# Kernel tuning notes

Hardware: AMD Instinct MI355X
Metric: run time of the kernel (lower is better)

Reference implementation:

```python
import jax, jax.numpy as jnp
import numpy as np


def setup_inputs() -> dict:
    key = jax.random.key(0)
    k_x, k_w = jax.random.split(key)
    S, B, D, H = 2048, 16, 1024, 1024
    X = jax.random.normal(k_x, (S, B, D), dtype=jnp.float32)
    hidden = jnp.zeros((B, H), dtype=jnp.float32)  # initial C_0
    W = jax.random.normal(k_w, (3 * H, D), dtype=jnp.float32) * 0.02
    b = jnp.zeros((3 * H,), dtype=jnp.float32)
    return {"X": X, "hidden": hidden, "W": W, "b": b}


def reference(X, hidden, W, b):
    # QRNNLayer forward, window=1, output_gate=True, zoneout off (eval).
    # Linear projection: [S,B,D] @ [D,3H] -> [S,B,3H]
    Y = jnp.einsum('sbd,hd->sbh', X, W) + b
    Z, F, O = jnp.split(Y, 3, axis=2)
    Z = jnp.tanh(Z)
    F = jax.nn.sigmoid(F)
    O = jax.nn.sigmoid(O)

    # ForgetMult fo-pool: C_t = F_t * Z_t + (1 - F_t) * C_{t-1}
    def step(c, fz):
        f, z = fz
        c = f * z + (1.0 - f) * c
        return c, c

    _, C = jax.lax.scan(step, hidden, (F, Z))  # C: [S,B,H]
    H_out = O * C
    return H_out, C[-1:, :, :]  # (H, last cell state [1,B,H])
```

## Files before the change

kernel.cpp:

```cpp
#include <hip/hip_runtime.h>
#include <hip/hip_bf16.h>
#include <cstdint>
#include <cstddef>

#define S_LEN 2048
#define BATCH 16
#define DIM   1024
#define HID   1024
#define M_TOT (S_LEN * BATCH)
#define N_TOT (3 * HID)
#define K_TOT DIM
#define NCHUNK 32
#define CHLEN (S_LEN / NCHUNK)

#define BM 256
#define BN 256
#define BK 64
#define NT (K_TOT / BK)
#define NITER (NT / 2)
#define GRID_M (M_TOT / BM)
#define GRID_N (N_TOT / BN)
#define NWG (GRID_M * GRID_N)

typedef __bf16 bf16x8 __attribute__((ext_vector_type(8)));
typedef float  f32x4  __attribute__((ext_vector_type(4)));

__device__ __forceinline__ unsigned short f2bf(float f) {
    unsigned int u = __float_as_uint(f);
    u += 0x7FFFu + ((u >> 16) & 1u);
    return (unsigned short)(u >> 16);
}
__device__ __forceinline__ float bf2f(unsigned int s) {
    return __uint_as_float(s << 16);
}
__device__ __forceinline__ float fast_sigmoid(float x) { return 1.0f / (1.0f + __expf(-x)); }
__device__ __forceinline__ float fast_tanh(float x)    { return 2.0f / (1.0f + __expf(-2.0f * x)) - 1.0f; }

__global__ void __launch_bounds__(256) cvt_f32_bf16(const float* __restrict__ in,
                                                    unsigned short* __restrict__ out, int n4) {
    int i = blockIdx.x * blockDim.x + threadIdx.x;
    const int stride = gridDim.x * blockDim.x;
    for (; i < n4; i += stride) {
        const float4 v = reinterpret_cast<const float4*>(in)[i];
        ushort4 o;
        o.x = f2bf(v.x); o.y = f2bf(v.y); o.z = f2bf(v.z); o.w = f2bf(v.w);
        reinterpret_cast<ushort4*>(out)[i] = o;
    }
}

#define GLOAD_LDS16(gp, lp)                                                         \
    __builtin_amdgcn_global_load_lds((__attribute__((address_space(1))) void*)(gp), \
                                     (__attribute__((address_space(3))) void*)(lp), 16, 0, 0)

__global__ void __launch_bounds__(512, 2)
gemm_gates(const unsigned short* __restrict__ Xb,
           const unsigned short* __restrict__ Wb,
           const float* __restrict__ bias,
           unsigned short* __restrict__ gates) {
    __shared__ __align__(16) unsigned short LDSbuf[4 * BM * BK];
#define AS(s) (LDSbuf + (s) * (BM * BK))
#define BS(s) (LDSbuf + 2 * (BM * BK) + (s) * (BN * BK))

    const int tid  = threadIdx.x;
    const int lane = tid & 63;
    const int wid  = tid >> 6;
    const int wm   = wid >> 2;
    const int wn   = wid & 3;
    const int lr   = lane & 15;
    const int lc   = (lane >> 4) & 3;

    const int swz = (blockIdx.x & 7) * (NWG / 8) + (blockIdx.x >> 3);
    const int bn = swz % GRID_N;
    const int bm = swz / GRID_N;

    const int srow  = tid >> 3;
    const int scolE = (((tid & 7) ^ ((tid >> 3) & 7)) << 3);
    const unsigned short* gAs = Xb + (size_t)(bm * BM + srow) * K_TOT + scolE;
    const unsigned short* gBs = Wb + (size_t)(bn * BN + srow) * K_TOT + scolE;

#define STAGE_A(T, q) GLOAD_LDS16(gAs + (size_t)(q) * 64 * K_TOT + (T) * BK, \
                                  AS((T) & 1) + (q) * 4096 + tid * 8)
#define STAGE_B(T, q) GLOAD_LDS16(gBs + (size_t)(q) * 64 * K_TOT + (T) * BK, \
                                  BS((T) & 1) + (q) * 4096 + tid * 8)

#define LDA(dst, s, mf, kw) do { const int _r = wm * 128 + (mf) * 16 + lr;            \
        dst = *reinterpret_cast<const bf16x8*>(                                        \
            AS(s) + _r * 64 + (((((kw) << 2) | lc) ^ (_r & 7)) << 3)); } while (0)
#define LDB(dst, s, nf, kw) do { const int _r = wn * 64 + (nf) * 16 + lr;             \
        dst = *reinterpret_cast<const bf16x8*>(                                        \
            BS(s) + _r * 64 + (((((kw) << 2) | lc) ^ (_r & 7)) << 3)); } while (0)

#define RD_A(s, MH) do { _Pragma("unroll") for (int mi = 0; mi < 4; ++mi) {           \
        LDA(a[mi][0], s, (MH) * 4 + mi, 0); LDA(a[mi][1], s, (MH) * 4 + mi, 1); } } while (0)
#define RD_B(dst, s, NH) do { _Pragma("unroll") for (int ni = 0; ni < 2; ++ni) {      \
        LDB(dst[ni][0], s, (NH) * 2 + ni, 0); LDB(dst[ni][1], s, (NH) * 2 + ni, 1); } } while (0)

#define MM16(A_, B_, M0, N0) do {                                                     \
    _Pragma("unroll") for (int mi = 0; mi < 4; ++mi)                                  \
    _Pragma("unroll") for (int ni = 0; ni < 2; ++ni) {                                \
        acc[(M0) + mi][(N0) + ni] = __builtin_amdgcn_mfma_f32_16x16x32_bf16(          \
            A_[mi][0], B_[ni][0], acc[(M0) + mi][(N0) + ni], 0, 0, 0);                \
        acc[(M0) + mi][(N0) + ni] = __builtin_amdgcn_mfma_f32_16x16x32_bf16(          \
            A_[mi][1], B_[ni][1], acc[(M0) + mi][(N0) + ni], 0, 0, 0);                \
    } } while (0)

#define BAR __builtin_amdgcn_s_barrier()
#define SP1 __builtin_amdgcn_s_setprio(1)
#define SP0 __builtin_amdgcn_s_setprio(0)

    f32x4 acc[8][4];
#pragma unroll
    for (int m = 0; m < 8; ++m)
#pragma unroll
        for (int n = 0; n < 4; ++n) acc[m][n] = {0.0f, 0.0f, 0.0f, 0.0f};

    bf16x8 a[4][2], b[2][2], b2[2][2];

    STAGE_A(0, 0); STAGE_A(0, 1); STAGE_A(0, 2); STAGE_A(0, 3);
    STAGE_B(0, 0); STAGE_B(0, 1); STAGE_B(0, 2); STAGE_B(0, 3);
    STAGE_A(1, 0); STAGE_A(1, 2);
    STAGE_B(1, 0); STAGE_B(1, 1);
    STAGE_A(1, 1); STAGE_A(1, 3);
    asm volatile("s_waitcnt vmcnt(6)" ::: "memory");
    BAR;

#pragma unroll 1
    for (int j = 0; j < NITER; ++j) {
        const int t0 = 2 * j;
        const int t1 = 2 * j + 1;
        const bool st = (j < NITER - 1);
        RD_A(0, 0); RD_B(b, 0, 0);
        STAGE_B(t1, 2); STAGE_B(t1, 3);
        BAR; SP1; MM16(a, b, 0, 0); SP0; BAR;
        RD_B(b2, 0, 1);
        if (st) { STAGE_A(t0 + 2, 0); STAGE_A(t0 + 2, 2); }
        BAR; SP1; MM16(a, b2, 0, 2); SP0; BAR;
        RD_A(0, 1);
        if (st) { STAGE_B(t0 + 2, 0); STAGE_B(t0 + 2, 1); }
        BAR; SP1; MM16(a, b, 4, 0); SP0; BAR;
        if (st) { STAGE_A(t0 + 2, 1); STAGE_A(t0 + 2, 3); }
        BAR; SP1; MM16(a, b2, 4, 2); SP0;
        if (st) asm volatile("s_waitcnt vmcnt(6)" ::: "memory");
        else    asm volatile("s_waitcnt vmcnt(0)" ::: "memory");
        BAR;
        RD_A(1, 0); RD_B(b, 1, 0);
        if (st) { STAGE_B(t0 + 2, 2); STAGE_B(t0 + 2, 3); }
        BAR; SP1; MM16(a, b, 0, 0); SP0; BAR;
        RD_B(b2, 1, 1);
        if (st) { STAGE_A(t1 + 2, 0); STAGE_A(t1 + 2, 2); }
        BAR; SP1; MM16(a, b2, 0, 2); SP0; BAR;
        RD_A(1, 1);
        if (st) { STAGE_B(t1 + 2, 0); STAGE_B(t1 + 2, 1); }
        BAR; SP1; MM16(a, b, 4, 0); SP0; BAR;
        if (st) { STAGE_A(t1 + 2, 1); STAGE_A(t1 + 2, 3); }
        BAR; SP1; MM16(a, b2, 4, 2); SP0;
        if (st) asm volatile("s_waitcnt vmcnt(6)" ::: "memory");
        BAR;
    }
#undef STAGE_A
#undef STAGE_B
#undef LDA
#undef LDB
#undef RD_A
#undef RD_B
#undef MM16
#undef BAR
#undef SP1
#undef SP0

    const int gate_id = bn >> 2;
    {
        const int rl0 = wm * 128 + ((lane >> 4) << 2);
        const int cl0 = wn * 64 + lr;
#pragma unroll
        for (int nf = 0; nf < 4; ++nf) {
            const int col = cl0 + nf * 16;
            const float bb = bias[bn * BN + col];
#pragma unroll
            for (int mf = 0; mf < 8; ++mf) {
#pragma unroll
                for (int r = 0; r < 4; ++r) {
                    const int row = rl0 + mf * 16 + r;
                    const float y = acc[mf][nf][r] + bb;
                    const float g = (gate_id == 0) ? fast_tanh(y) : fast_sigmoid(y);
                    const int phys = (col >> 3) ^ (row & 7);
                    LDSbuf[row * 256 + (phys << 3) + (col & 7)] = f2bf(g);
                }
            }
        }
    }
    __syncthreads();
    {
        const int gr  = lane & 31;
        const int rsub = lane >> 5;
#pragma unroll
        for (int i = 0; i < 16; ++i) {
            const int rl  = wid * 32 + i * 2 + rsub;
            const int phys = gr ^ (rl & 7);
            const bf16x8 v = *reinterpret_cast<const bf16x8*>(&LDSbuf[rl * 256 + (phys << 3)]);
            *reinterpret_cast<bf16x8*>(&gates[(size_t)(bm * BM + rl) * N_TOT + bn * BN + gr * 8]) = v;
        }
    }
#undef AS
#undef BS
}

__global__ void __launch_bounds__(256) scan_phase1(const unsigned short* __restrict__ gates,
                                                   float* __restrict__ Aprod,
                                                   float* __restrict__ Cend) {
    const int t = blockIdx.x * 256 + threadIdx.x;
    const int hp = t & 511;
    const int b  = (t >> 9) & (BATCH - 1);
    const int chunk = t >> 13;
    float c0 = 0.f, c1 = 0.f, a0 = 1.f, a1 = 1.f;
    const int m0 = chunk * (CHLEN * BATCH) + b;
    const unsigned short* gz = gates + (size_t)m0 * N_TOT + hp * 2;
#pragma unroll 4
    for (int i = 0; i < CHLEN; ++i) {
        const unsigned short* p = gz + (size_t)i * BATCH * N_TOT;
        const unsigned int zz = *reinterpret_cast<const unsigned int*>(p);
        const unsigned int ff = *reinterpret_cast<const unsigned int*>(p + HID);
        const float z0 = bf2f(zz & 0xffffu), z1 = bf2f(zz >> 16);
        const float f0 = bf2f(ff & 0xffffu), f1 = bf2f(ff >> 16);
        const float o0 = 1.f - f0, o1 = 1.f - f1;
        c0 = f0 * z0 + o0 * c0;  c1 = f1 * z1 + o1 * c1;
        a0 *= o0;                a1 *= o1;
    }
    const int idx = chunk * (BATCH * HID) + b * HID + hp * 2;
    *reinterpret_cast<float2*>(&Aprod[idx]) = make_float2(a0, a1);
    *reinterpret_cast<float2*>(&Cend[idx])  = make_float2(c0, c1);
}

__global__ void __launch_bounds__(256) scan_combine(const float* __restrict__ Aprod,
                                                    const float* __restrict__ Cend,
                                                    const float* __restrict__ hidden,
                                                    float* __restrict__ Cstart,
                                                    float* __restrict__ c_last) {
    const int t = blockIdx.x * 256 + threadIdx.x;
    float c = hidden[t];
#pragma unroll
    for (int j = 0; j < NCHUNK; ++j) {
        const int idx = j * (BATCH * HID) + t;
        Cstart[idx] = c;
        c = Aprod[idx] * c + Cend[idx];
    }
    c_last[t] = c;
}

__global__ void __launch_bounds__(256) scan_phase3(const unsigned short* __restrict__ gates,
                                                   const float* __restrict__ Cstart,
                                                   float* __restrict__ Hout) {
    const int t = blockIdx.x * 256 + threadIdx.x;
    const int hp = t & 511;
    const int b  = (t >> 9) & (BATCH - 1);
    const int chunk = t >> 13;
    const int idx = chunk * (BATCH * HID) + b * HID + hp * 2;
    float2 cs = *reinterpret_cast<const float2*>(&Cstart[idx]);
    float c0 = cs.x, c1 = cs.y;
    const int m0 = chunk * (CHLEN * BATCH) + b;
    const unsigned short* gz = gates + (size_t)m0 * N_TOT + hp * 2;
#pragma unroll 4
    for (int i = 0; i < CHLEN; ++i) {
        const unsigned short* p = gz + (size_t)i * BATCH * N_TOT;
        const unsigned int zz = *reinterpret_cast<const unsigned int*>(p);
        const unsigned int ff = *reinterpret_cast<const unsigned int*>(p + HID);
        const unsigned int oo = *reinterpret_cast<const unsigned int*>(p + 2 * HID);
        const float z0 = bf2f(zz & 0xffffu), z1 = bf2f(zz >> 16);
        const float f0 = bf2f(ff & 0xffffu), f1 = bf2f(ff >> 16);
        const float g0 = bf2f(oo & 0xffffu), g1 = bf2f(oo >> 16);
        c0 = f0 * z0 + (1.f - f0) * c0;
        c1 = f1 * z1 + (1.f - f1) * c1;
        const int m = m0 + i * BATCH;
        *reinterpret_cast<float2*>(&Hout[(size_t)m * HID + hp * 2]) = make_float2(g0 * c0, g1 * c1);
    }
}

extern "C" void kernel_launch(void* const* d_in, const int* in_sizes, int n_in,
                              void* d_out, int out_size, void* d_ws, size_t ws_size,
                              hipStream_t stream) {
    const float* X      = (const float*)d_in[0];
    const float* hidden = (const float*)d_in[1];
    const float* W      = (const float*)d_in[2];
    const float* bias   = (const float*)d_in[3];
    float* out    = (float*)d_out;
    float* c_last = out + (size_t)M_TOT * HID;

    char* ws = (char*)d_ws;
    unsigned short* Xb    = (unsigned short*)ws;
    unsigned short* Wb    = (unsigned short*)(ws + (size_t)M_TOT * K_TOT * 2);
    unsigned short* gates = Wb + (size_t)N_TOT * K_TOT;
    float* Aprod  = (float*)(gates + (size_t)M_TOT * N_TOT);
    float* Cend   = Aprod + (size_t)NCHUNK * BATCH * HID;
    float* Cstart = Cend  + (size_t)NCHUNK * BATCH * HID;

    cvt_f32_bf16<<<dim3(2048), dim3(256), 0, stream>>>(X, Xb, (int)(M_TOT * K_TOT / 4));
    cvt_f32_bf16<<<dim3(512),  dim3(256), 0, stream>>>(W, Wb, (int)(N_TOT * K_TOT / 4));
    gemm_gates<<<dim3(NWG), dim3(512), 0, stream>>>(Xb, Wb, bias, gates);
    scan_phase1<<<dim3(1024), dim3(256), 0, stream>>>(gates, Aprod, Cend);
    scan_combine<<<dim3(64), dim3(256), 0, stream>>>(Aprod, Cend, hidden, Cstart, c_last);
    scan_phase3<<<dim3(1024), dim3(256), 0, stream>>>(gates, Cstart, out);
}
```

Measured before the change: 387.5 us.

## Switch GEMM to 32x32x16 MFMA, two-pass epilogue, and fuse bf16 conversions

Replaces the 16x16x32 bf16 MFMA tiling with 32x32x16 MFMA fragments, cutting the number of MFMA issues and LDS fragment reads per K step. The epilogue is reworked to match the 32x32 accumulator layout and runs in two passes of 128 rows through LDS, one per warp-row group. The two f32-to-bf16 conversion launches are merged into one kernel to save a launch. The change also leaves behind a dead first epilogue loop that computes activations and discards them, and the two-pass write-out adds barriers.

```diff
diff --git a/kernel.cpp b/kernel.cpp
--- a/kernel.cpp
+++ b/kernel.cpp
@@ -23,7 +23,7 @@
 #define NWG (GRID_M * GRID_N)
 
 typedef __bf16 bf16x8 __attribute__((ext_vector_type(8)));
-typedef float  f32x4  __attribute__((ext_vector_type(4)));
+typedef float  f32x16 __attribute__((ext_vector_type(16)));
 
 __device__ __forceinline__ unsigned short f2bf(float f) {
     unsigned int u = __float_as_uint(f);
@@ -36,15 +36,24 @@
 __device__ __forceinline__ float fast_sigmoid(float x) { return 1.0f / (1.0f + __expf(-x)); }
 __device__ __forceinline__ float fast_tanh(float x)    { return 2.0f / (1.0f + __expf(-2.0f * x)) - 1.0f; }
 
-__global__ void __launch_bounds__(256) cvt_f32_bf16(const float* __restrict__ in,
-                                                    unsigned short* __restrict__ out, int n4) {
-    int i = blockIdx.x * blockDim.x + threadIdx.x;
-    const int stride = gridDim.x * blockDim.x;
-    for (; i < n4; i += stride) {
-        const float4 v = reinterpret_cast<const float4*>(in)[i];
-        ushort4 o;
-        o.x = f2bf(v.x); o.y = f2bf(v.y); o.z = f2bf(v.z); o.w = f2bf(v.w);
-        reinterpret_cast<ushort4*>(out)[i] = o;
+__global__ void __launch_bounds__(256) cvt_both(const float* __restrict__ X,
+                                                const float* __restrict__ W,
+                                                unsigned short* __restrict__ Xb,
+                                                unsigned short* __restrict__ Wb) {
+    const int nx = (M_TOT * K_TOT) / 4;
+    const int nw = (N_TOT * K_TOT) / 4;
+    if (blockIdx.x < 2048) {
+        for (int i = blockIdx.x * 256 + threadIdx.x; i < nx; i += 2048 * 256) {
+            const float4 v = reinterpret_cast<const float4*>(X)[i];
+            ushort4 o; o.x = f2bf(v.x); o.y = f2bf(v.y); o.z = f2bf(v.z); o.w = f2bf(v.w);
+            reinterpret_cast<ushort4*>(Xb)[i] = o;
+        }
+    } else {
+        for (int i = (blockIdx.x - 2048) * 256 + threadIdx.x; i < nw; i += 512 * 256) {
+            const float4 v = reinterpret_cast<const float4*>(W)[i];
+            ushort4 o; o.x = f2bf(v.x); o.y = f2bf(v.y); o.z = f2bf(v.z); o.w = f2bf(v.w);
+            reinterpret_cast<ushort4*>(Wb)[i] = o;
+        }
     }
 }
 
@@ -66,8 +75,8 @@
     const int wid  = tid >> 6;
     const int wm   = wid >> 2;
     const int wn   = wid & 3;
-    const int lr   = lane & 15;
-    const int lc   = (lane >> 4) & 3;
+    const int l31  = lane & 31;
+    const int lhi  = lane >> 5;
 
     const int swz = (blockIdx.x & 7) * (NWG / 8) + (blockIdx.x >> 3);
     const int bn = swz % GRID_N;
@@ -83,38 +92,38 @@
 #define STAGE_B(T, q) GLOAD_LDS16(gBs + (size_t)(q) * 64 * K_TOT + (T) * BK, \
                                   BS((T) & 1) + (q) * 4096 + tid * 8)
 
-#define LDA(dst, s, mf, kw) do { const int _r = wm * 128 + (mf) * 16 + lr;            \
+#define LDA(dst, s, mf, ks) do { const int _r = wm * 128 + (mf) * 32 + l31;           \
         dst = *reinterpret_cast<const bf16x8*>(                                        \
-            AS(s) + _r * 64 + (((((kw) << 2) | lc) ^ (_r & 7)) << 3)); } while (0)
-#define LDB(dst, s, nf, kw) do { const int _r = wn * 64 + (nf) * 16 + lr;             \
+            AS(s) + _r * 64 + (((((ks) << 1) | lhi) ^ (_r & 7)) << 3)); } while (0)
+#define LDB(dst, s, nf, ks) do { const int _r = wn * 64 + (nf) * 32 + l31;            \
         dst = *reinterpret_cast<const bf16x8*>(                                        \
-            BS(s) + _r * 64 + (((((kw) << 2) | lc) ^ (_r & 7)) << 3)); } while (0)
-
-#define RD_A(s, MH) do { _Pragma("unroll") for (int mi = 0; mi < 4; ++mi) {           \
-        LDA(a[mi][0], s, (MH) * 4 + mi, 0); LDA(a[mi][1], s, (MH) * 4 + mi, 1); } } while (0)
-#define RD_B(dst, s, NH) do { _Pragma("unroll") for (int ni = 0; ni < 2; ++ni) {      \
-        LDB(dst[ni][0], s, (NH) * 2 + ni, 0); LDB(dst[ni][1], s, (NH) * 2 + ni, 1); } } while (0)
-
-#define MM16(A_, B_, M0, N0) do {                                                     \
-    _Pragma("unroll") for (int mi = 0; mi < 4; ++mi)                                  \
-    _Pragma("unroll") for (int ni = 0; ni < 2; ++ni) {                                \
-        acc[(M0) + mi][(N0) + ni] = __builtin_amdgcn_mfma_f32_16x16x32_bf16(          \
-            A_[mi][0], B_[ni][0], acc[(M0) + mi][(N0) + ni], 0, 0, 0);                \
-        acc[(M0) + mi][(N0) + ni] = __builtin_amdgcn_mfma_f32_16x16x32_bf16(          \
-            A_[mi][1], B_[ni][1], acc[(M0) + mi][(N0) + ni], 0, 0, 0);                \
-    } } while (0)
+            BS(s) + _r * 64 + (((((ks) << 1) | lhi) ^ (_r & 7)) << 3)); } while (0)
+
+#define RD_A(s, MH) do { _Pragma("unroll") for (int mi = 0; mi < 2; ++mi)             \
+        _Pragma("unroll") for (int ks = 0; ks < 4; ++ks)                              \
+            LDA(a[mi][ks], s, (MH) * 2 + mi, ks); } while (0)
+#define RD_B(dst, s, NF) do { _Pragma("unroll") for (int ks = 0; ks < 4; ++ks)        \
+        LDB(dst[ks], s, NF, ks); } while (0)
+
+#define MM32(A_, B_, MH, NF) do {                                                     \
+    _Pragma("unroll") for (int mi = 0; mi < 2; ++mi)                                  \
+    _Pragma("unroll") for (int ks = 0; ks < 4; ++ks)                                  \
+        acc[(MH) * 2 + mi][NF] = __builtin_amdgcn_mfma_f32_32x32x16_bf16(             \
+            A_[mi][ks], B_[ks], acc[(MH) * 2 + mi][NF], 0, 0, 0); } while (0)
 
 #define BAR __builtin_amdgcn_s_barrier()
 #define SP1 __builtin_amdgcn_s_setprio(1)
 #define SP0 __builtin_amdgcn_s_setprio(0)
 
-    f32x4 acc[8][4];
-#pragma unroll
-    for (int m = 0; m < 8; ++m)
-#pragma unroll
-        for (int n = 0; n < 4; ++n) acc[m][n] = {0.0f, 0.0f, 0.0f, 0.0f};
-
-    bf16x8 a[4][2], b[2][2], b2[2][2];
+    f32x16 acc[4][2];
+#pragma unroll
+    for (int m = 0; m < 4; ++m)
+#pragma unroll
+        for (int n = 0; n < 2; ++n)
+#pragma unroll
+            for (int r = 0; r < 16; ++r) acc[m][n][r] = 0.0f;
+
+    bf16x8 a[2][4], b[4], b2[4];
 
     STAGE_A(0, 0); STAGE_A(0, 1); STAGE_A(0, 2); STAGE_A(0, 3);
     STAGE_B(0, 0); STAGE_B(0, 1); STAGE_B(0, 2); STAGE_B(0, 3);
@@ -131,29 +140,29 @@
         const bool st = (j < NITER - 1);
         RD_A(0, 0); RD_B(b, 0, 0);
         STAGE_B(t1, 2); STAGE_B(t1, 3);
-        BAR; SP1; MM16(a, b, 0, 0); SP0; BAR;
+        BAR; SP1; MM32(a, b, 0, 0); SP0; BAR;
         RD_B(b2, 0, 1);
         if (st) { STAGE_A(t0 + 2, 0); STAGE_A(t0 + 2, 2); }
-        BAR; SP1; MM16(a, b2, 0, 2); SP0; BAR;
+        BAR; SP1; MM32(a, b2, 0, 1); SP0; BAR;
         RD_A(0, 1);
         if (st) { STAGE_B(t0 + 2, 0); STAGE_B(t0 + 2, 1); }
-        BAR; SP1; MM16(a, b, 4, 0); SP0; BAR;
+        BAR; SP1; MM32(a, b, 1, 0); SP0; BAR;
         if (st) { STAGE_A(t0 + 2, 1); STAGE_A(t0 + 2, 3); }
-        BAR; SP1; MM16(a, b2, 4, 2); SP0;
+        BAR; SP1; MM32(a, b2, 1, 1); SP0;
         if (st) asm volatile("s_waitcnt vmcnt(6)" ::: "memory");
         else    asm volatile("s_waitcnt vmcnt(0)" ::: "memory");
         BAR;
         RD_A(1, 0); RD_B(b, 1, 0);
         if (st) { STAGE_B(t0 + 2, 2); STAGE_B(t0 + 2, 3); }
-        BAR; SP1; MM16(a, b, 0, 0); SP0; BAR;
+        BAR; SP1; MM32(a, b, 0, 0); SP0; BAR;
         RD_B(b2, 1, 1);
         if (st) { STAGE_A(t1 + 2, 0); STAGE_A(t1 + 2, 2); }
-        BAR; SP1; MM16(a, b2, 0, 2); SP0; BAR;
+        BAR; SP1; MM32(a, b2, 0, 1); SP0; BAR;
         RD_A(1, 1);
         if (st) { STAGE_B(t1 + 2, 0); STAGE_B(t1 + 2, 1); }
-        BAR; SP1; MM16(a, b, 4, 0); SP0; BAR;
+        BAR; SP1; MM32(a, b, 1, 0); SP0; BAR;
         if (st) { STAGE_A(t1 + 2, 1); STAGE_A(t1 + 2, 3); }
-        BAR; SP1; MM16(a, b2, 4, 2); SP0;
+        BAR; SP1; MM32(a, b2, 1, 1); SP0;
         if (st) asm volatile("s_waitcnt vmcnt(6)" ::: "memory");
         BAR;
     }
@@ -163,46 +172,76 @@
 #undef LDB
 #undef RD_A
 #undef RD_B
-#undef MM16
+#undef MM32
+
+    const int gate_id = bn >> 2;
+    {
+        const int cl0 = wn * 64;
+#pragma unroll
+        for (int nf = 0; nf < 2; ++nf) {
+            const int col = cl0 + nf * 32 + l31;
+            const float bb = bias[bn * BN + col];
+#pragma unroll
+            for (int mf = 0; mf < 4; ++mf) {
+#pragma unroll
+                for (int r = 0; r < 16; ++r) {
+                    const int row = wm * 128 + mf * 32 + (r & 3) + 8 * (r >> 2) + 4 * lhi;
+                    const float y = acc[mf][nf][r] + bb;
+                    const float g = (gate_id == 0) ? fast_tanh(y) : fast_sigmoid(y);
+                    const int rl = row & 127;
+                    const int phys = (col >> 3) ^ (rl & 7);
+                    if (false) {}
+                    else {
+                    }
+                }
+            }
+        }
+    }
+    const int gr   = lane & 31;
+    const int rsub = lane >> 5;
+#pragma unroll
+    for (int p = 0; p < 2; ++p) {
+        if (wm == p) {
+            const int cl0 = wn * 64;
+#pragma unroll
+            for (int nf = 0; nf < 2; ++nf) {
+                const int col = cl0 + nf * 32 + l31;
+                const float bb = bias[bn * BN + col];
+#pragma unroll
+                for (int mf = 0; mf < 4; ++mf) {
+#pragma unroll
+                    for (int r = 0; r < 16; ++r) {
+                        const int rl = mf * 32 + (r & 3) + 8 * (r >> 2) + 4 * lhi;
+                        const float y = acc[mf][nf][r] + bb;
+                        const float g = (gate_id == 0) ? fast_tanh(y) : fast_sigmoid(y);
+                        const int phys = (col >> 3) ^ (rl & 7);
+                        LDSbuf[rl * 256 + (phys << 3) + (col & 7)] = f2bf(g);
+                    }
+                }
+            }
+        }
+        asm volatile("s_waitcnt lgkmcnt(0)" ::: "memory");
+        __builtin_amdgcn_sched_barrier(0);
+        __builtin_amdgcn_s_barrier();
+#pragma unroll
+        for (int i = 0; i < 8; ++i) {
+            const int rl = wid * 16 + i * 2 + rsub;
+            const int phys = gr ^ (rl & 7);
+            const bf16x8 v = *reinterpret_cast<const bf16x8*>(&LDSbuf[rl * 256 + (phys << 3)]);
+            *reinterpret_cast<bf16x8*>(
+                &gates[(size_t)(bm * BM + p * 128 + rl) * N_TOT + bn * BN + gr * 8]) = v;
+        }
+        if (p == 0) {
+            asm volatile("s_waitcnt lgkmcnt(0)" ::: "memory");
+            __builtin_amdgcn_sched_barrier(0);
+            __builtin_amdgcn_s_barrier();
+        }
+    }
+#undef AS
+#undef BS
 #undef BAR
 #undef SP1
 #undef SP0
-
-    const int gate_id = bn >> 2;
-    {
-        const int rl0 = wm * 128 + ((lane >> 4) << 2);
-        const int cl0 = wn * 64 + lr;
-#pragma unroll
-        for (int nf = 0; nf < 4; ++nf) {
-            const int col = cl0 + nf * 16;
-            const float bb = bias[bn * BN + col];
-#pragma unroll
-            for (int mf = 0; mf < 8; ++mf) {
-#pragma unroll
-                for (int r = 0; r < 4; ++r) {
-                    const int row = rl0 + mf * 16 + r;
-                    const float y = acc[mf][nf][r] + bb;
-                    const float g = (gate_id == 0) ? fast_tanh(y) : fast_sigmoid(y);
-                    const int phys = (col >> 3) ^ (row & 7);
-                    LDSbuf[row * 256 + (phys << 3) + (col & 7)] = f2bf(g);
-                }
-            }
-        }
-    }
-    __syncthreads();
-    {
-        const int gr  = lane & 31;
-        const int rsub = lane >> 5;
-#pragma unroll
-        for (int i = 0; i < 16; ++i) {
-            const int rl  = wid * 32 + i * 2 + rsub;
-            const int phys = gr ^ (rl & 7);
-            const bf16x8 v = *reinterpret_cast<const bf16x8*>(&LDSbuf[rl * 256 + (phys << 3)]);
-            *reinterpret_cast<bf16x8*>(&gates[(size_t)(bm * BM + rl) * N_TOT + bn * BN + gr * 8]) = v;
-        }
-    }
-#undef AS
-#undef BS
 }
 
 __global__ void __launch_bounds__(256) scan_phase1(const unsigned short* __restrict__ gates,
@@ -293,8 +332,7 @@
     float* Cend   = Aprod + (size_t)NCHUNK * BATCH * HID;
     float* Cstart = Cend  + (size_t)NCHUNK * BATCH * HID;
 
-    cvt_f32_bf16<<<dim3(2048), dim3(256), 0, stream>>>(X, Xb, (int)(M_TOT * K_TOT / 4));
-    cvt_f32_bf16<<<dim3(512),  dim3(256), 0, stream>>>(W, Wb, (int)(N_TOT * K_TOT / 4));
+    cvt_both<<<dim3(2560), dim3(256), 0, stream>>>(X, W, Xb, Wb);
     gemm_gates<<<dim3(NWG), dim3(512), 0, stream>>>(Xb, Wb, bias, gates);
     scan_phase1<<<dim3(1024), dim3(256), 0, stream>>>(gates, Aprod, Cend);
     scan_combine<<<dim3(64), dim3(256), 0, stream>>>(Aprod, Cend, hidden, Cstart, c_last);
```

Measured after the change: 446.9 us. +15.3%, slower.
